# Kernel optimization log

Hardware: AMD Instinct MI355X
Metric: run time of the kernel (lower is better)

The kernel has to match this reference:

```python
import jax, jax.numpy as jnp
import numpy as np

D = 1024
H = 16
HD = D // H


def setup_inputs() -> dict:
    key = jax.random.key(0)
    ks = jax.random.split(key, 5)
    s = 1.0 / np.sqrt(D)
    return {
        "inputs": jax.random.normal(ks[0], (2, 2048, D), dtype=jnp.float32),
        "Wq": jax.random.normal(ks[1], (D, D), dtype=jnp.float32) * s,
        "bq": jnp.zeros((D,), jnp.float32),
        "Wk": jax.random.normal(ks[2], (D, D), dtype=jnp.float32) * s,
        "bk": jnp.zeros((D,), jnp.float32),
        "Wv": jax.random.normal(ks[3], (D, D), dtype=jnp.float32) * s,
        "bv": jnp.zeros((D,), jnp.float32),
        "Wo": jax.random.normal(ks[4], (D, D), dtype=jnp.float32) * s,
        "bo": jnp.zeros((D,), jnp.float32),
    }


def reference(inputs, Wq, bq, Wk, bk, Wv, bv, Wo, bo):
    B, S, _ = inputs.shape
    def split_heads(x):  # [B,S,D] -> [B,H,S,hd]
        return x.reshape(B, S, H, HD).transpose(0, 2, 1, 3)
    q = split_heads(inputs @ Wq + bq)
    k = split_heads(inputs @ Wk + bk)
    v = split_heads(inputs @ Wv + bv)
    scale = 1.0 / jnp.sqrt(jnp.asarray(HD, inputs.dtype))
    scores = jnp.einsum("bhsd,bhtd->bhst", q, k) * scale  # [B,H,S,S]
    weights = jax.nn.softmax(scores, axis=-1)
    attn = jnp.einsum("bhst,bhtd->bhsd", weights, v)
    concat = attn.transpose(0, 2, 1, 3).reshape(B, S, D)
    return concat @ Wo + bo
```

## Files before the change

### kernel.cpp

```cpp
#include <hip/hip_runtime.h>


typedef __bf16 bf16x8 __attribute__((ext_vector_type(8)));
typedef float  f32x4  __attribute__((ext_vector_type(4)));

#if __has_builtin(__builtin_amdgcn_exp2f)
#define EXPFN(x) __builtin_amdgcn_exp2f(x)
#define QSCALE (0.125f * 1.44269504088896f)
#else
#define EXPFN(x) __expf(x)
#define QSCALE 0.125f
#endif

#define VMCNT(n)  asm volatile("s_waitcnt vmcnt(" #n ")" ::: "memory")
#define LGKMCNT0() asm volatile("s_waitcnt lgkmcnt(0)" ::: "memory")
#define BARRIER() __builtin_amdgcn_s_barrier()
#define WAIT0_BARRIER() asm volatile("s_waitcnt vmcnt(0)\n\ts_barrier" ::: "memory")

__device__ __forceinline__ unsigned short f2bf(float f) {
    unsigned int u = __float_as_uint(f);
    u += 0x7FFFu + ((u >> 16) & 1u);
    return (unsigned short)(u >> 16);
}

__device__ __forceinline__ void gload16(const void* g, void* l) {
    __builtin_amdgcn_global_load_lds(
        (const __attribute__((address_space(1))) void*)g,
        (__attribute__((address_space(3))) void*)l, 16, 0, 0);
}

__global__ __launch_bounds__(256) void prep_kernel(
    const float* __restrict__ X, ushort4* __restrict__ Xb,
    const float* __restrict__ Wq, const float* __restrict__ Wk,
    const float* __restrict__ Wv, const float* __restrict__ Wo,
    unsigned short* __restrict__ Wt_all) {
    const int z = blockIdx.z;
    if (z == 4) {
        int base = (blockIdx.y * 32 + blockIdx.x) * 1024 + threadIdx.x;
        const float4* X4 = (const float4*)X;
        #pragma unroll
        for (int c = 0; c < 4; c++) {
            int i = base + c * 256;
            float4 v = X4[i];
            ushort4 o;
            o.x = f2bf(v.x); o.y = f2bf(v.y); o.z = f2bf(v.z); o.w = f2bf(v.w);
            Xb[i] = o;
        }
        return;
    }
    __shared__ float tile[32][33];
    const float* W = (z == 0) ? Wq : (z == 1) ? Wk : (z == 2) ? Wv : Wo;
    unsigned short* Wt = Wt_all + (size_t)z * 1024 * 1024;
    int c0 = blockIdx.x * 32, r0 = blockIdx.y * 32;
    int x = threadIdx.x & 31, y = threadIdx.x >> 5;
    for (int j = 0; j < 32; j += 8)
        tile[y + j][x] = W[(r0 + y + j) * 1024 + c0 + x];
    __syncthreads();
    for (int j = 0; j < 32; j += 8)
        Wt[(c0 + y + j) * 1024 + r0 + x] = f2bf(tile[x][y + j]);
}

__global__ __launch_bounds__(256, 2) void gemm_qkv_kernel(
    const unsigned short* __restrict__ Xb, const unsigned short* __restrict__ Wt_all,
    const float* __restrict__ bq, const float* __restrict__ bk,
    const float* __restrict__ bv,
    unsigned short* __restrict__ Qb, unsigned short* __restrict__ Kb,
    unsigned short* __restrict__ Vt) {
    const int x0 = blockIdx.x * 128;
    const int y0 = blockIdx.y * 64;

    __shared__ __align__(16) unsigned short smem[128 * 64 + 3 * 64 * 64];
    unsigned short* As  = smem;
    unsigned short* Bqs = smem + 8192;
    unsigned short* Bks = smem + 12288;
    unsigned short* Bvs = smem + 16384;

    const unsigned short* Ap  = Xb + (size_t)x0 * 1024;
    const unsigned short* Bqp = Wt_all + (size_t)y0 * 1024;
    const unsigned short* Bkp = Wt_all + 1048576u + (size_t)y0 * 1024;
    const unsigned short* Bvp = Wt_all + 2097152u + (size_t)y0 * 1024;

    const int tid = threadIdx.x;
    const int lane = tid & 63, wave = tid >> 6;
    const int quad = lane >> 4, l15 = lane & 15;
    const int wrow = (wave >> 1) * 64, wcol = (wave & 1) * 32;

    f32x4 aq[4][2] = {};
    f32x4 ak[4][2] = {};
    f32x4 av[4][2] = {};

    const int srow = lane >> 3;
    const int ch8  = (lane & 7) * 8;
    const int swz  = (((lane & 7) ^ srow)) * 8;
    const int sw   = (l15 & 7);

    for (int k0 = 0; k0 < 1024; k0 += 64) {
        #pragma unroll
        for (int c = 0; c < 4; c++) {
            int r = c * 32 + wave * 8 + srow;
            gload16(Ap + (size_t)r * 1024 + k0 + swz, &As[r * 64 + ch8]);
        }
        #pragma unroll
        for (int c = 0; c < 2; c++) {
            int r = c * 32 + wave * 8 + srow;
            gload16(Bqp + (size_t)r * 1024 + k0 + swz, &Bqs[r * 64 + ch8]);
            gload16(Bkp + (size_t)r * 1024 + k0 + swz, &Bks[r * 64 + ch8]);
            gload16(Bvp + (size_t)r * 1024 + k0 + swz, &Bvs[r * 64 + ch8]);
        }
        WAIT0_BARRIER();
        #pragma unroll
        for (int kk = 0; kk < 2; kk++) {
            bf16x8 af[4], bqf[2], bkf[2], bvf[2];
            const int co = (((kk * 4 + quad) ^ sw)) * 8;
            #pragma unroll
            for (int i = 0; i < 4; i++)
                af[i] = *(const bf16x8*)&As[(wrow + i * 16 + l15) * 64 + co];
            #pragma unroll
            for (int j = 0; j < 2; j++) {
                bqf[j] = *(const bf16x8*)&Bqs[(wcol + j * 16 + l15) * 64 + co];
                bkf[j] = *(const bf16x8*)&Bks[(wcol + j * 16 + l15) * 64 + co];
                bvf[j] = *(const bf16x8*)&Bvs[(wcol + j * 16 + l15) * 64 + co];
            }
            #pragma unroll
            for (int i = 0; i < 4; i++)
                #pragma unroll
                for (int j = 0; j < 2; j++) {
                    aq[i][j] = __builtin_amdgcn_mfma_f32_16x16x32_bf16(
                        af[i], bqf[j], aq[i][j], 0, 0, 0);
                    ak[i][j] = __builtin_amdgcn_mfma_f32_16x16x32_bf16(
                        af[i], bkf[j], ak[i][j], 0, 0, 0);
                    av[i][j] = __builtin_amdgcn_mfma_f32_16x16x32_bf16(
                        af[i], bvf[j], av[i][j], 0, 0, 0);
                }
        }
        __syncthreads();
    }

    #pragma unroll
    for (int j = 0; j < 2; j++) {
        int col = y0 + wcol + j * 16 + l15;
        float bqc = bq[col], bkc = bk[col];
        int h = col >> 6, d = col & 63;
        #pragma unroll
        for (int i = 0; i < 4; i++)
            #pragma unroll
            for (int r = 0; r < 4; r++) {
                int row = x0 + wrow + i * 16 + quad * 4 + r;
                int b = row >> 11, s = row & 2047;
                size_t idx = (size_t)((b * 16 + h) * 2048 + s) * 64 + d;
                Qb[idx] = f2bf((aq[i][j][r] + bqc) * QSCALE);
                Kb[idx] = f2bf(ak[i][j][r] + bkc);
            }
    }

    __syncthreads();
    unsigned short* vts = smem;
    #pragma unroll
    for (int j = 0; j < 2; j++) {
        int n = wcol + j * 16 + l15;
        float bvc = bv[y0 + n];
        #pragma unroll
        for (int i = 0; i < 4; i++)
            #pragma unroll
            for (int r = 0; r < 4; r++) {
                int m = wrow + i * 16 + quad * 4 + r;
                vts[n * 136 + m] = f2bf(av[i][j][r] + bvc);
            }
    }
    __syncthreads();
    const int bseq = x0 >> 11;
    const int s0 = x0 & 2047;
    #pragma unroll
    for (int q = 0; q < 4; q++) {
        int c = q * 256 + tid;
        int n = c >> 4, mc = c & 15;
        uint4 vv = *(const uint4*)&vts[n * 136 + mc * 8];
        *(uint4*)&Vt[(size_t)(bseq * 1024 + y0 + n) * 2048 + s0 + mc * 8] = vv;
    }
}

__global__ __launch_bounds__(256) void attn_kernel(
    const unsigned short* __restrict__ Qb, const unsigned short* __restrict__ Kb,
    const unsigned short* __restrict__ Vt, unsigned short* __restrict__ Cc,
    float* __restrict__ Op, float* __restrict__ Lp, int tlen, int do_split) {
    const int bh = blockIdx.y;
    const int b = bh >> 4, h = bh & 15;
    const int q0 = blockIdx.x * 128;
    const int split = blockIdx.z;
    const int tbeg = split * tlen;

    const int tid = threadIdx.x;
    const int lane = tid & 63, wave = tid >> 6;
    const int quad = lane >> 4, l15 = lane & 15;

    __shared__ __align__(16) unsigned short Ks[2][64 * 64];
    __shared__ __align__(16) unsigned short Vs[2][64 * 64];

    const unsigned short* Qbh = Qb + (size_t)bh * 2048 * 64;
    const unsigned short* Kbh = Kb + (size_t)bh * 2048 * 64;
    const unsigned short* Vbh = Vt + (size_t)bh * 64 * 2048;

    bf16x8 qa[2][2];
    #pragma unroll
    for (int mi = 0; mi < 2; mi++)
        #pragma unroll
        for (int kk = 0; kk < 2; kk++)
            qa[mi][kk] = *(const bf16x8*)&Qbh[
                (size_t)(q0 + wave * 32 + mi * 16 + l15) * 64 + kk * 32 + quad * 8];

    union { unsigned short us[8]; bf16x8 v; } ones_u;
    #pragma unroll
    for (int i = 0; i < 8; i++) ones_u.us[i] = 0x3F80;
    const bf16x8 onesv = ones_u.v;

    f32x4 o[2][4] = {};
    f32x4 ol[2] = {};

    const int srow = lane >> 3;
    const int r0s = wave * 16 + srow;
    const int ch8 = (lane & 7) * 8;
    const int swz = (((lane & 7) ^ srow)) * 8;
    const int sw  = (l15 & 7);

    const int pk0 = (r0s & 0x23) | ((r0s & 0x0C) << 1) | ((r0s & 0x10) >> 2);
    const int r8  = r0s + 8;
    const int pk8 = (r8 & 0x23) | ((r8 & 0x0C) << 1) | ((r8 & 0x10) >> 2);

    auto stage = [&](int buf, int t0) {
        gload16(&Kbh[(size_t)(t0 + pk0) * 64 + swz],       &Ks[buf][r0s * 64 + ch8]);
        gload16(&Kbh[(size_t)(t0 + pk8) * 64 + swz],       &Ks[buf][(r0s + 8) * 64 + ch8]);
        gload16(&Vbh[(size_t)r0s * 2048 + t0 + swz],       &Vs[buf][r0s * 64 + ch8]);
        gload16(&Vbh[(size_t)(r0s + 8) * 2048 + t0 + swz], &Vs[buf][(r0s + 8) * 64 + ch8]);
    };

    stage(0, tbeg);
    int cur = 0;
    for (int ti = 0; ti < tlen; ti += 64) {
        VMCNT(0);
        LGKMCNT0();
        BARRIER();
        if (ti + 64 < tlen)
            stage(cur ^ 1, tbeg + ti + 64);
        const unsigned short* Ksc = Ks[cur];
        const unsigned short* Vsc = Vs[cur];

        f32x4 sf[2][4] = {};
        #pragma unroll
        for (int j = 0; j < 4; j++)
            #pragma unroll
            for (int kk = 0; kk < 2; kk++) {
                bf16x8 kf = *(const bf16x8*)&Ksc[(j * 16 + l15) * 64 +
                                                 (((kk * 4 + quad) ^ sw)) * 8];
                sf[0][j] = __builtin_amdgcn_mfma_f32_16x16x32_bf16(kf, qa[0][kk], sf[0][j], 0, 0, 0);
                sf[1][j] = __builtin_amdgcn_mfma_f32_16x16x32_bf16(kf, qa[1][kk], sf[1][j], 0, 0, 0);
            }

        union { unsigned int u[4]; bf16x8 v; } pa[2][2];
        #pragma unroll
        for (int mi = 0; mi < 2; mi++) {
            float pe[4][4];
            #pragma unroll
            for (int j = 0; j < 4; j++)
                #pragma unroll
                for (int r = 0; r < 4; r++)
                    pe[j][r] = EXPFN(sf[mi][j][r]);
            #pragma unroll
            for (int kk = 0; kk < 2; kk++)
                #pragma unroll
                for (int d = 0; d < 4; d++) {
                    const int j = 2 * kk + (d >> 1);
                    const int r = 2 * (d & 1);
                    unsigned int w;
                    asm("v_cvt_pk_bf16_f32 %0, %1, %2"
                        : "=v"(w) : "v"(pe[j][r]), "v"(pe[j][r + 1]));
                    pa[mi][kk].u[d] = w;
                }
        }

        #pragma unroll
        for (int kk = 0; kk < 2; kk++) {
            bf16x8 pf0 = pa[0][kk].v;
            bf16x8 pf1 = pa[1][kk].v;
            ol[0] = __builtin_amdgcn_mfma_f32_16x16x32_bf16(pf0, onesv, ol[0], 0, 0, 0);
            ol[1] = __builtin_amdgcn_mfma_f32_16x16x32_bf16(pf1, onesv, ol[1], 0, 0, 0);
            #pragma unroll
            for (int j = 0; j < 4; j++) {
                bf16x8 vf = *(const bf16x8*)&Vsc[(j * 16 + l15) * 64 +
                                                 (((kk * 4 + quad) ^ sw)) * 8];
                o[0][j] = __builtin_amdgcn_mfma_f32_16x16x32_bf16(pf0, vf, o[0][j], 0, 0, 0);
                o[1][j] = __builtin_amdgcn_mfma_f32_16x16x32_bf16(pf1, vf, o[1][j], 0, 0, 0);
            }
        }
        cur ^= 1;
    }

    if (do_split) {
        float* Opd = Op + (size_t)(split * 32 + bh) * 2048 * 64;
        float* Lpd = Lp + (size_t)(split * 32 + bh) * 2048;
        #pragma unroll
        for (int mi = 0; mi < 2; mi++)
            #pragma unroll
            for (int r = 0; r < 4; r++) {
                int s = q0 + wave * 32 + mi * 16 + quad * 4 + r;
                if (l15 == 0) Lpd[s] = ol[mi][r];
                #pragma unroll
                for (int j = 0; j < 4; j++)
                    Opd[(size_t)s * 64 + j * 16 + l15] = o[mi][j][r];
            }
    } else {
        #pragma unroll
        for (int mi = 0; mi < 2; mi++)
            #pragma unroll
            for (int r = 0; r < 4; r++) {
                float inv = 1.f / ol[mi][r];
                int s = q0 + wave * 32 + mi * 16 + quad * 4 + r;
                size_t row = (size_t)(b * 2048 + s);
                #pragma unroll
                for (int j = 0; j < 4; j++)
                    Cc[row * 1024 + h * 64 + j * 16 + l15] = f2bf(o[mi][j][r] * inv);
            }
    }
}

__global__ __launch_bounds__(256) void combine_kernel(
    const float4* __restrict__ Op, const float* __restrict__ Lp,
    unsigned short* __restrict__ Cc) {
    int idx = blockIdx.x * 256 + threadIdx.x;
    int d4 = idx & 15;
    int s = (idx >> 4) & 2047;
    int bh = idx >> 15;
    const size_t half4 = (size_t)32 * 2048 * 16;
    float4 a = Op[(size_t)idx], c = Op[half4 + (size_t)idx];
    float l = Lp[bh * 2048 + s] + Lp[32 * 2048 + bh * 2048 + s];
    float inv = 1.f / l;
    ushort4 o;
    o.x = f2bf((a.x + c.x) * inv); o.y = f2bf((a.y + c.y) * inv);
    o.z = f2bf((a.z + c.z) * inv); o.w = f2bf((a.w + c.w) * inv);
    int b = bh >> 4, h = bh & 15;
    *(ushort4*)&Cc[((size_t)(b * 2048 + s)) * 1024 + h * 64 + d4 * 4] = o;
}

__global__ __launch_bounds__(256) void gemm_out_kernel(
    const unsigned short* __restrict__ Cc, const unsigned short* __restrict__ Wot,
    const float* __restrict__ bo, float* __restrict__ out) {
    const int m0 = blockIdx.x * 128;
    const int n0 = blockIdx.y * 64;

    __shared__ __align__(16) unsigned short As[128 * 64];
    __shared__ __align__(16) unsigned short Bs[64 * 64];

    const int tid = threadIdx.x;
    const int lane = tid & 63, wave = tid >> 6;
    const int quad = lane >> 4, l15 = lane & 15;
    const int wrow = (wave >> 1) * 64, wcol = (wave & 1) * 32;

    f32x4 acc[4][2] = {};
    const int srow = lane >> 3;
    const int ch8 = (lane & 7) * 8;
    const int swz = (((lane & 7) ^ srow)) * 8;
    const int sw  = (l15 & 7);

    for (int k0 = 0; k0 < 1024; k0 += 64) {
        #pragma unroll
        for (int c = 0; c < 4; c++) {
            int r = c * 32 + wave * 8 + srow;
            gload16(Cc + (size_t)(m0 + r) * 1024 + k0 + swz, &As[r * 64 + ch8]);
            if (c < 2)
                gload16(Wot + (size_t)(n0 + r) * 1024 + k0 + swz, &Bs[r * 64 + ch8]);
        }
        WAIT0_BARRIER();
        #pragma unroll
        for (int kk = 0; kk < 2; kk++) {
            bf16x8 af[4], bfr[2];
            #pragma unroll
            for (int i = 0; i < 4; i++)
                af[i] = *(const bf16x8*)&As[(wrow + i * 16 + l15) * 64 +
                                            (((kk * 4 + quad) ^ sw)) * 8];
            #pragma unroll
            for (int j = 0; j < 2; j++)
                bfr[j] = *(const bf16x8*)&Bs[(wcol + j * 16 + l15) * 64 +
                                             (((kk * 4 + quad) ^ sw)) * 8];
            #pragma unroll
            for (int i = 0; i < 4; i++)
                #pragma unroll
                for (int j = 0; j < 2; j++)
                    acc[i][j] = __builtin_amdgcn_mfma_f32_16x16x32_bf16(
                        af[i], bfr[j], acc[i][j], 0, 0, 0);
        }
        __syncthreads();
    }

    #pragma unroll
    for (int j = 0; j < 2; j++) {
        int col = n0 + wcol + j * 16 + l15;
        float bcol = bo[col];
        #pragma unroll
        for (int i = 0; i < 4; i++)
            #pragma unroll
            for (int r = 0; r < 4; r++) {
                int row = m0 + wrow + i * 16 + quad * 4 + r;
                out[(size_t)row * 1024 + col] = acc[i][j][r] + bcol;
            }
    }
}

extern "C" void kernel_launch(void* const* d_in, const int* in_sizes, int n_in,
                              void* d_out, int out_size, void* d_ws, size_t ws_size,
                              hipStream_t stream) {
    const float* X  = (const float*)d_in[0];
    const float* Wq = (const float*)d_in[1];
    const float* bq = (const float*)d_in[2];
    const float* Wk = (const float*)d_in[3];
    const float* bk = (const float*)d_in[4];
    const float* Wv = (const float*)d_in[5];
    const float* bv = (const float*)d_in[6];
    const float* Wo = (const float*)d_in[7];
    const float* bo = (const float*)d_in[8];
    float* out = (float*)d_out;

    char* ws = (char*)d_ws;
    unsigned short* Xb = (unsigned short*)(ws);
    unsigned short* Wt = (unsigned short*)(ws + (8u  << 20));
    unsigned short* Qb = (unsigned short*)(ws + (16u << 20));
    unsigned short* Kb = (unsigned short*)(ws + (24u << 20));
    unsigned short* Vt = (unsigned short*)(ws + (32u << 20));
    unsigned short* Cc = (unsigned short*)(ws + (40u << 20));
    float* Op = (float*)(ws + (48u << 20));
    float* Lp = (float*)(ws + (48u << 20) + 33554432u);
    const bool use_split = ws_size >= ((size_t)(48u << 20) + 33554432u + 524288u);

    prep_kernel<<<dim3(32, 32, 5), 256, 0, stream>>>(X, (ushort4*)Xb, Wq, Wk, Wv, Wo, Wt);
    gemm_qkv_kernel<<<dim3(32, 16), 256, 0, stream>>>(Xb, Wt, bq, bk, bv, Qb, Kb, Vt);
    if (use_split) {
        attn_kernel<<<dim3(16, 32, 2), 256, 0, stream>>>(Qb, Kb, Vt, Cc, Op, Lp, 1024, 1);
        combine_kernel<<<4096, 256, 0, stream>>>((const float4*)Op, Lp, Cc);
    } else {
        attn_kernel<<<dim3(16, 32, 1), 256, 0, stream>>>(Qb, Kb, Vt, Cc, Op, Lp, 2048, 0);
    }
    gemm_out_kernel<<<dim3(32, 16), 256, 0, stream>>>(Cc, Wt + 3u * 1024 * 1024, bo, out);
}
```

Before: 184.3 us.

## Software-pipeline attention loop: compute next QK tile while doing exp and PV

Restructures the attention inner loop so the QK^T MFMAs for tile i+1 are issued after tile i's exponentials and before its PV MFMAs. Loads are now staged two tiles ahead, with K double-buffered and V triple-buffered in LDS. The aim is to overlap the exp/convert work with matrix-core work and to hide global load latency. In exchange it uses more LDS and registers for the second score buffer. The loop is unrolled by two and assumes the tile count is even.

```diff
diff --git a/kernel.cpp b/kernel.cpp
--- a/kernel.cpp
+++ b/kernel.cpp
@@ -194,7 +194,7 @@
     const int quad = lane >> 4, l15 = lane & 15;
 
     __shared__ __align__(16) unsigned short Ks[2][64 * 64];
-    __shared__ __align__(16) unsigned short Vs[2][64 * 64];
+    __shared__ __align__(16) unsigned short Vs[3][64 * 64];
 
     const unsigned short* Qbh = Qb + (size_t)bh * 2048 * 64;
     const unsigned short* Kbh = Kb + (size_t)bh * 2048 * 64;
@@ -226,57 +226,63 @@
     const int r8  = r0s + 8;
     const int pk8 = (r8 & 0x23) | ((r8 & 0x0C) << 1) | ((r8 & 0x10) >> 2);
 
-    auto stage = [&](int buf, int t0) {
-        gload16(&Kbh[(size_t)(t0 + pk0) * 64 + swz],       &Ks[buf][r0s * 64 + ch8]);
-        gload16(&Kbh[(size_t)(t0 + pk8) * 64 + swz],       &Ks[buf][(r0s + 8) * 64 + ch8]);
-        gload16(&Vbh[(size_t)r0s * 2048 + t0 + swz],       &Vs[buf][r0s * 64 + ch8]);
-        gload16(&Vbh[(size_t)(r0s + 8) * 2048 + t0 + swz], &Vs[buf][(r0s + 8) * 64 + ch8]);
+    auto stage = [&](int i) {
+        const int t0 = tbeg + i * 64;
+        unsigned short* Kd = Ks[i & 1];
+        unsigned short* Vd = Vs[i % 3];
+        gload16(&Kbh[(size_t)(t0 + pk0) * 64 + swz],       &Kd[r0s * 64 + ch8]);
+        gload16(&Kbh[(size_t)(t0 + pk8) * 64 + swz],       &Kd[(r0s + 8) * 64 + ch8]);
+        gload16(&Vbh[(size_t)r0s * 2048 + t0 + swz],       &Vd[r0s * 64 + ch8]);
+        gload16(&Vbh[(size_t)(r0s + 8) * 2048 + t0 + swz], &Vd[(r0s + 8) * 64 + ch8]);
     };
 
-    stage(0, tbeg);
-    int cur = 0;
-    for (int ti = 0; ti < tlen; ti += 64) {
-        VMCNT(0);
-        LGKMCNT0();
-        BARRIER();
-        if (ti + 64 < tlen)
-            stage(cur ^ 1, tbeg + ti + 64);
-        const unsigned short* Ksc = Ks[cur];
-        const unsigned short* Vsc = Vs[cur];
-
-        f32x4 sf[2][4] = {};
+    auto qk_tile = [&](int i, f32x4 (&sfN)[2][4]) {
+        const unsigned short* Ksc = Ks[i & 1];
+        #pragma unroll
+        for (int mi = 0; mi < 2; mi++)
+            #pragma unroll
+            for (int j = 0; j < 4; j++)
+                sfN[mi][j] = (f32x4){0.f, 0.f, 0.f, 0.f};
         #pragma unroll
         for (int j = 0; j < 4; j++)
             #pragma unroll
             for (int kk = 0; kk < 2; kk++) {
                 bf16x8 kf = *(const bf16x8*)&Ksc[(j * 16 + l15) * 64 +
                                                  (((kk * 4 + quad) ^ sw)) * 8];
-                sf[0][j] = __builtin_amdgcn_mfma_f32_16x16x32_bf16(kf, qa[0][kk], sf[0][j], 0, 0, 0);
-                sf[1][j] = __builtin_amdgcn_mfma_f32_16x16x32_bf16(kf, qa[1][kk], sf[1][j], 0, 0, 0);
-            }
-
+                sfN[0][j] = __builtin_amdgcn_mfma_f32_16x16x32_bf16(kf, qa[0][kk], sfN[0][j], 0, 0, 0);
+                sfN[1][j] = __builtin_amdgcn_mfma_f32_16x16x32_bf16(kf, qa[1][kk], sfN[1][j], 0, 0, 0);
+            }
+    };
+
+    const int NT = tlen >> 6;
+
+    auto iter_body = [&](int i, f32x4 (&sfC)[2][4], f32x4 (&sfN)[2][4]) {
         union { unsigned int u[4]; bf16x8 v; } pa[2][2];
         #pragma unroll
-        for (int mi = 0; mi < 2; mi++) {
-            float pe[4][4];
-            #pragma unroll
-            for (int j = 0; j < 4; j++)
-                #pragma unroll
-                for (int r = 0; r < 4; r++)
-                    pe[j][r] = EXPFN(sf[mi][j][r]);
+        for (int mi = 0; mi < 2; mi++)
             #pragma unroll
             for (int kk = 0; kk < 2; kk++)
                 #pragma unroll
                 for (int d = 0; d < 4; d++) {
                     const int j = 2 * kk + (d >> 1);
                     const int r = 2 * (d & 1);
+                    float e0 = EXPFN(sfC[mi][j][r]);
+                    float e1 = EXPFN(sfC[mi][j][r + 1]);
                     unsigned int w;
                     asm("v_cvt_pk_bf16_f32 %0, %1, %2"
-                        : "=v"(w) : "v"(pe[j][r]), "v"(pe[j][r + 1]));
+                        : "=v"(w) : "v"(e0), "v"(e1));
                     pa[mi][kk].u[d] = w;
                 }
-        }
-
+
+        VMCNT(0);
+        LGKMCNT0();
+        BARRIER();
+
+        if (i + 2 < NT) stage(i + 2);
+
+        if (i + 1 < NT) qk_tile(i + 1, sfN);
+
+        const unsigned short* Vsc = Vs[i % 3];
         #pragma unroll
         for (int kk = 0; kk < 2; kk++) {
             bf16x8 pf0 = pa[0][kk].v;
@@ -291,7 +297,19 @@
                 o[1][j] = __builtin_amdgcn_mfma_f32_16x16x32_bf16(pf1, vf, o[1][j], 0, 0, 0);
             }
         }
-        cur ^= 1;
+    };
+
+    f32x4 sfA[2][4], sfB[2][4];
+    stage(0);
+    VMCNT(0);
+    BARRIER();
+    stage(1);
+    qk_tile(0, sfA);
+
+    for (int ti = 0; ti < tlen; ti += 128) {
+        const int i = ti >> 6;
+        iter_body(i,     sfA, sfB);
+        iter_body(i + 1, sfB, sfA);
     }
 
     if (do_split) {
```

New measurement: 188.0 us. 2.0% more time.

## Double-buffer LDS tiles in QKV and output projection GEMMs

Applied to the files above, without the earlier changes.

Both projection GEMMs now use two LDS buffers. The next K-tile is issued via global_load_lds right after the barrier, so it loads while MFMAs run on the current tile. This removes the per-iteration trailing __syncthreads and is meant to hide global load latency behind compute. The cost is double the LDS use (80KB for the QKV kernel), which may lower occupancy below the requested 2 blocks per CU. The vmcnt(0) wait at the top of each iteration still waits for the prefetch issued one iteration earlier.

```diff
diff --git a/kernel.cpp b/kernel.cpp
--- a/kernel.cpp
+++ b/kernel.cpp
@@ -15,7 +15,6 @@
 #define VMCNT(n)  asm volatile("s_waitcnt vmcnt(" #n ")" ::: "memory")
 #define LGKMCNT0() asm volatile("s_waitcnt lgkmcnt(0)" ::: "memory")
 #define BARRIER() __builtin_amdgcn_s_barrier()
-#define WAIT0_BARRIER() asm volatile("s_waitcnt vmcnt(0)\n\ts_barrier" ::: "memory")
 
 __device__ __forceinline__ unsigned short f2bf(float f) {
     unsigned int u = __float_as_uint(f);
@@ -69,11 +68,7 @@
     const int x0 = blockIdx.x * 128;
     const int y0 = blockIdx.y * 64;
 
-    __shared__ __align__(16) unsigned short smem[128 * 64 + 3 * 64 * 64];
-    unsigned short* As  = smem;
-    unsigned short* Bqs = smem + 8192;
-    unsigned short* Bks = smem + 12288;
-    unsigned short* Bvs = smem + 16384;
+    __shared__ __align__(16) unsigned short smem[2][20480];
 
     const unsigned short* Ap  = Xb + (size_t)x0 * 1024;
     const unsigned short* Bqp = Wt_all + (size_t)y0 * 1024;
@@ -94,7 +89,11 @@
     const int swz  = (((lane & 7) ^ srow)) * 8;
     const int sw   = (l15 & 7);
 
-    for (int k0 = 0; k0 < 1024; k0 += 64) {
+    auto stage = [&](int buf, int k0) {
+        unsigned short* As  = smem[buf];
+        unsigned short* Bqs = smem[buf] + 8192;
+        unsigned short* Bks = smem[buf] + 12288;
+        unsigned short* Bvs = smem[buf] + 16384;
         #pragma unroll
         for (int c = 0; c < 4; c++) {
             int r = c * 32 + wave * 8 + srow;
@@ -107,7 +106,20 @@
             gload16(Bkp + (size_t)r * 1024 + k0 + swz, &Bks[r * 64 + ch8]);
             gload16(Bvp + (size_t)r * 1024 + k0 + swz, &Bvs[r * 64 + ch8]);
         }
-        WAIT0_BARRIER();
+    };
+
+    stage(0, 0);
+    int cur = 0;
+    for (int k0 = 0; k0 < 1024; k0 += 64) {
+        VMCNT(0);
+        LGKMCNT0();
+        BARRIER();
+        if (k0 + 64 < 1024)
+            stage(cur ^ 1, k0 + 64);
+        const unsigned short* As  = smem[cur];
+        const unsigned short* Bqs = smem[cur] + 8192;
+        const unsigned short* Bks = smem[cur] + 12288;
+        const unsigned short* Bvs = smem[cur] + 16384;
         #pragma unroll
         for (int kk = 0; kk < 2; kk++) {
             bf16x8 af[4], bqf[2], bkf[2], bvf[2];
@@ -133,7 +145,7 @@
                         af[i], bvf[j], av[i][j], 0, 0, 0);
                 }
         }
-        __syncthreads();
+        cur ^= 1;
     }
 
     #pragma unroll
@@ -154,7 +166,7 @@
     }
 
     __syncthreads();
-    unsigned short* vts = smem;
+    unsigned short* vts = smem[0];
     #pragma unroll
     for (int j = 0; j < 2; j++) {
         int n = wcol + j * 16 + l15;
@@ -346,8 +358,8 @@
     const int m0 = blockIdx.x * 128;
     const int n0 = blockIdx.y * 64;
 
-    __shared__ __align__(16) unsigned short As[128 * 64];
-    __shared__ __align__(16) unsigned short Bs[64 * 64];
+    __shared__ __align__(16) unsigned short As[2][128 * 64];
+    __shared__ __align__(16) unsigned short Bs[2][64 * 64];
 
     const int tid = threadIdx.x;
     const int lane = tid & 63, wave = tid >> 6;
@@ -360,26 +372,35 @@
     const int swz = (((lane & 7) ^ srow)) * 8;
     const int sw  = (l15 & 7);
 
-    for (int k0 = 0; k0 < 1024; k0 += 64) {
+    auto stage = [&](int buf, int k0) {
         #pragma unroll
         for (int c = 0; c < 4; c++) {
             int r = c * 32 + wave * 8 + srow;
-            gload16(Cc + (size_t)(m0 + r) * 1024 + k0 + swz, &As[r * 64 + ch8]);
+            gload16(Cc + (size_t)(m0 + r) * 1024 + k0 + swz, &As[buf][r * 64 + ch8]);
             if (c < 2)
-                gload16(Wot + (size_t)(n0 + r) * 1024 + k0 + swz, &Bs[r * 64 + ch8]);
-        }
-        WAIT0_BARRIER();
+                gload16(Wot + (size_t)(n0 + r) * 1024 + k0 + swz, &Bs[buf][r * 64 + ch8]);
+        }
+    };
+
+    stage(0, 0);
+    int cur = 0;
+    for (int k0 = 0; k0 < 1024; k0 += 64) {
+        VMCNT(0);
+        LGKMCNT0();
+        BARRIER();
+        if (k0 + 64 < 1024)
+            stage(cur ^ 1, k0 + 64);
         #pragma unroll
         for (int kk = 0; kk < 2; kk++) {
             bf16x8 af[4], bfr[2];
             #pragma unroll
             for (int i = 0; i < 4; i++)
-                af[i] = *(const bf16x8*)&As[(wrow + i * 16 + l15) * 64 +
-                                            (((kk * 4 + quad) ^ sw)) * 8];
+                af[i] = *(const bf16x8*)&As[cur][(wrow + i * 16 + l15) * 64 +
+                                                 (((kk * 4 + quad) ^ sw)) * 8];
             #pragma unroll
             for (int j = 0; j < 2; j++)
-                bfr[j] = *(const bf16x8*)&Bs[(wcol + j * 16 + l15) * 64 +
-                                             (((kk * 4 + quad) ^ sw)) * 8];
+                bfr[j] = *(const bf16x8*)&Bs[cur][(wcol + j * 16 + l15) * 64 +
+                                                  (((kk * 4 + quad) ^ sw)) * 8];
             #pragma unroll
             for (int i = 0; i < 4; i++)
                 #pragma unroll
@@ -387,7 +408,7 @@
                     acc[i][j] = __builtin_amdgcn_mfma_f32_16x16x32_bf16(
                         af[i], bfr[j], acc[i][j], 0, 0, 0);
         }
-        __syncthreads();
+        cur ^= 1;
     }
 
     #pragma unroll
```

Result: no change. 184.5 us, median of 3 (+0.1%).
